# Kernel optimization log

Measured on AMD Instinct MI355X. Metric: run time of the kernel, lower is better.

The kernel has to match this reference:

```python
import jax, jax.numpy as jnp
import numpy as np

N, T, FS, FD, GH, RH, E = 100000, 24, 32, 8, 32, 64, 3200000


def spmm(edge_row, edge_col, edge_val, X):
    # out[i] = sum_e val[e] * X[col[e]]  for edges with row[e]==i
    return jax.ops.segment_sum(edge_val[:, None] * X[edge_col], edge_row, num_segments=N)


def setup_inputs() -> dict:
    key = jax.random.key(0)
    ks = jax.random.split(key, 20)
    s = 0.05
    return {
        "X_static": jax.random.normal(ks[0], (N, FS), jnp.float32),
        "X_dyn_mean": jax.random.normal(ks[1], (T, N, FD), jnp.float32),
        "edge_row": jax.random.randint(ks[2], (E,), 0, N, jnp.int32),
        "edge_col": jax.random.randint(ks[3], (E,), 0, N, jnp.int32),
        "edge_val": jax.random.uniform(ks[4], (E,), jnp.float32),
        # GraphConv layers
        "g1_W": jax.random.normal(ks[5], (GH, FS), jnp.float32) * s,
        "g1_b": jnp.zeros((GH,), jnp.float32),
        "g2_W": jax.random.normal(ks[6], (GH, GH), jnp.float32) * s,
        "g2_b": jnp.zeros((GH,), jnp.float32),
        # GRU (PyTorch layout: 3H rows = [r, z, n])
        "W_ih": jax.random.normal(ks[7], (3 * RH, GH + FD), jnp.float32) * s,
        "W_hh": jax.random.normal(ks[8], (3 * RH, RH), jnp.float32) * s,
        "b_ih": jnp.zeros((3 * RH,), jnp.float32),
        "b_hh": jnp.zeros((3 * RH,), jnp.float32),
        # MLP head
        "h1_W": jax.random.normal(ks[9], (64, RH), jnp.float32) * s,
        "h1_b": jnp.zeros((64,), jnp.float32),
        "h2_W": jax.random.normal(ks[10], (1, 64), jnp.float32) * s,
        "h2_b": jnp.zeros((1,), jnp.float32),
    }


def reference(X_static, X_dyn_mean, edge_row, edge_col, edge_val,
              g1_W, g1_b, g2_W, g2_b, W_ih, W_hh, b_ih, b_hh,
              h1_W, h1_b, h2_W, h2_b):
    # GraphConv x2: linear then sparse A_hat @ Xw, ReLU
    h = jax.nn.relu(spmm(edge_row, edge_col, edge_val, X_static @ g1_W.T + g1_b))
    h = jax.nn.relu(spmm(edge_row, edge_col, edge_val, h @ g2_W.T + g2_b))  # (N, GH)

    # z_t = concat([h, X_dyn_mean[t]], -1); precompute input-gate projections
    z_seq = jnp.concatenate([jnp.broadcast_to(h[None], (T, N, GH)), X_dyn_mean], axis=-1)  # (T,N,GH+FD)
    gi_all = jnp.einsum('tnd,hd->tnh', z_seq, W_ih) + b_ih  # (T,N,3H)

    def step(hs, gi):
        gh = hs @ W_hh.T + b_hh
        i_r, i_z, i_n = jnp.split(gi, 3, axis=-1)
        h_r, h_z, h_n = jnp.split(gh, 3, axis=-1)
        r = jax.nn.sigmoid(i_r + h_r)
        zg = jax.nn.sigmoid(i_z + h_z)
        n = jnp.tanh(i_n + r * h_n)
        h_new = (1.0 - zg) * n + zg * hs
        return h_new, h_new

    h0 = jnp.zeros((N, RH), jnp.float32)
    _, out = jax.lax.scan(step, h0, gi_all)  # (T,N,RH)

    y = jax.nn.relu(out @ h1_W.T + h1_b)
    y = jax.nn.sigmoid(y @ h2_W.T + h2_b)[..., 0]  # (T,N)
    return y
```

## Files before the change

### kernel.cpp

```cpp
#include <hip/hip_runtime.h>
#include <math.h>

typedef short bf16x8_t __attribute__((ext_vector_type(8)));
typedef float f32x4_t  __attribute__((ext_vector_type(4)));

__device__ __forceinline__ float fast_rcp(float x) { return __builtin_amdgcn_rcpf(x); }
__device__ __forceinline__ float sigmoidf_(float x) {
  return fast_rcp(1.0f + __expf(-x));
}
__device__ __forceinline__ float tanhf_(float x) {
  return fmaf(-2.0f, fast_rcp(__expf(2.0f * x) + 1.0f), 1.0f);
}
__device__ __forceinline__ unsigned short f2bf(float f) {
  unsigned int u = __float_as_uint(f);
  unsigned int r = (u + 0x7fffu + ((u >> 16) & 1u)) >> 16;
  return (unsigned short)r;
}
__device__ __forceinline__ float bf2f(unsigned short u) {
  return __uint_as_float(((unsigned int)u) << 16);
}
__device__ __forceinline__ unsigned int cvt_pk_bf16(float a, float b) {
  unsigned int d;
  asm("v_cvt_pk_bf16_f32 %0, %1, %2" : "=v"(d) : "v"(a), "v"(b));
  return d;
}

template<bool RELU_IN, bool OUT_BF16>
__global__ __launch_bounds__(256) void lin32_kernel(
    const float* __restrict__ X, const float* __restrict__ W,
    const float* __restrict__ b, void* __restrict__ outp, int N)
{
  __shared__ float sW[32][33];
  __shared__ float sb[32];
  __shared__ float sX[8][33];
  const int tid = threadIdx.x;
  for (int i = tid; i < 1024; i += 256) sW[i >> 5][i & 31] = W[i];
  if (tid < 32) sb[tid] = b[tid];
  const int n0 = blockIdx.x * 8;
  {
    float v = X[(size_t)n0 * 32 + tid];
    if (RELU_IN) v = fmaxf(v, 0.0f);
    sX[tid >> 5][tid & 31] = v;
  }
  __syncthreads();
  const int ln = tid >> 5, f = tid & 31;
  float acc = sb[f];
  #pragma unroll
  for (int j = 0; j < 32; j++) acc += sX[ln][j] * sW[f][j];
  if (OUT_BF16) ((unsigned short*)outp)[(size_t)n0 * 32 + tid] = f2bf(acc);
  else          ((float*)outp)[(size_t)n0 * 32 + tid] = acc;
}

__global__ __launch_bounds__(256) void spmm_kernel(
    const int* __restrict__ erow, const int* __restrict__ ecol,
    const float* __restrict__ eval, const float* __restrict__ X,
    float* __restrict__ out, int E)
{
  const long gid = (long)blockIdx.x * 256 + threadIdx.x;
  const int e = (int)(gid >> 3);
  const int q = (int)(gid & 7);
  if (e >= E) return;
  const int r = erow[e], c = ecol[e];
  const float v = eval[e];
  const float4 x = *(const float4*)(X + (size_t)c * 32 + q * 4);
  float* o = out + (size_t)r * 32 + q * 4;
  atomicAdd(o + 0, v * x.x);
  atomicAdd(o + 1, v * x.y);
  atomicAdd(o + 2, v * x.z);
  atomicAdd(o + 3, v * x.w);
}

#define BROWS 128
#define BSHIFT 7
#define EPB 4096
#define MAXBUCKETS 1024

__global__ __launch_bounds__(256) void lin_hist_k(
    const float* __restrict__ X, const float* __restrict__ W,
    const float* __restrict__ b, unsigned short* __restrict__ outp,
    int N, int linBlocks,
    const int* __restrict__ erow, int* __restrict__ blockHist,
    int* __restrict__ blockCnt, int E, int nBuckets)
{
  __shared__ float sW[32][33];
  __shared__ float sb[32];
  __shared__ float sX[8][33];
  __shared__ int h[MAXBUCKETS];
  const int tid = threadIdx.x;
  if ((int)blockIdx.x < linBlocks) {
    for (int i = tid; i < 1024; i += 256) sW[i >> 5][i & 31] = W[i];
    if (tid < 32) sb[tid] = b[tid];
    const int n0 = blockIdx.x * 8;
    sX[tid >> 5][tid & 31] = X[(size_t)n0 * 32 + tid];
    __syncthreads();
    const int ln = tid >> 5, f = tid & 31;
    float acc = sb[f];
    #pragma unroll
    for (int j = 0; j < 32; j++) acc += sX[ln][j] * sW[f][j];
    outp[(size_t)n0 * 32 + tid] = f2bf(acc);
  } else {
    const int bid = blockIdx.x - linBlocks;
    for (int i = tid; i < nBuckets; i += 256) h[i] = 0;
    __syncthreads();
    const int e0 = bid * EPB;
    const int cnt = min(E - e0, EPB);
    for (int i = tid; i < cnt; i += 256)
      atomicAdd(&h[erow[e0 + i] >> BSHIFT], 1);
    __syncthreads();
    int* o = blockHist + (size_t)bid * nBuckets;
    int* c = blockCnt + (size_t)bid * nBuckets;
    for (int i = tid; i < nBuckets; i += 256) { int v = h[i]; o[i] = v; c[i] = v; }
  }
}

__global__ __launch_bounds__(128) void colscan_k(
    int* __restrict__ blockHist, int* __restrict__ bucketTotal,
    int nb, int nBuckets)
{
  __shared__ int s[128];
  const int b = blockIdx.x;
  const int t = threadIdx.x;
  const int k = (nb + 127) >> 7;
  const int i0 = t * k, i1 = min(nb, i0 + k);
  int p = 0;
  for (int i = i0; i < i1; i++) p += blockHist[(size_t)i * nBuckets + b];
  s[t] = p;
  __syncthreads();
  #pragma unroll
  for (int off = 1; off < 128; off <<= 1) {
    int u = (t >= off) ? s[t - off] : 0;
    __syncthreads(); s[t] += u; __syncthreads();
  }
  int run = s[t] - p;
  if (t == 127) bucketTotal[b] = s[127];
  for (int i = i0; i < i1; i++) {
    int* q = &blockHist[(size_t)i * nBuckets + b];
    int v = *q;
    *q = run;
    run += v;
  }
}

__global__ __launch_bounds__(1024) void bucketstart_k(
    const int* __restrict__ bucketTotal, int* __restrict__ bucketStart,
    int nBuckets)
{
  __shared__ int s[1024];
  const int b = threadIdx.x;
  int v = (b < nBuckets) ? bucketTotal[b] : 0;
  s[b] = v;
  __syncthreads();
  for (int off = 1; off < 1024; off <<= 1) {
    int u = (b >= off) ? s[b - off] : 0;
    __syncthreads(); s[b] += u; __syncthreads();
  }
  if (b < nBuckets) bucketStart[b] = s[b] - v;
  if (b == nBuckets - 1) bucketStart[nBuckets] = s[b];
}

__global__ __launch_bounds__(256) void scatter_stage_k(
    const int* __restrict__ erow, const int* __restrict__ ecol,
    const float* __restrict__ evl, const int* __restrict__ blockOfs,
    const int* __restrict__ blockCnt,
    const int* __restrict__ bucketStart, int2* __restrict__ binned,
    int E, int nBuckets)
{
  __shared__ int2 rec[EPB];
  __shared__ unsigned short dstv[EPB];
  __shared__ int  cur[MAXBUCKETS];
  __shared__ int  gb[MAXBUCKETS];
  __shared__ int  part[256];
  const int tid = threadIdx.x;
  const int e0 = blockIdx.x * EPB;
  const int cntE = min(E - e0, EPB);
  const int* ofs = blockOfs + (size_t)blockIdx.x * nBuckets;
  const int* cnr = blockCnt + (size_t)blockIdx.x * nBuckets;

  for (int i = tid; i < nBuckets; i += 256) cur[i] = cnr[i];
  __syncthreads();

  const int k = (nBuckets + 255) >> 8;
  const int i0 = tid * k, i1 = min(i0 + k, nBuckets);
  int s = 0;
  for (int i = i0; i < i1; i++) s += cur[i];
  part[tid] = s;
  __syncthreads();
  for (int off = 1; off < 256; off <<= 1) {
    int u = (tid >= off) ? part[tid - off] : 0;
    __syncthreads(); part[tid] += u; __syncthreads();
  }
  int run = part[tid] - s;
  for (int i = i0; i < i1; i++) {
    int hv = cur[i];
    gb[i] = bucketStart[i] + ofs[i] - run;
    cur[i] = run;
    run += hv;
  }
  __syncthreads();

  for (int i = tid; i < cntE; i += 256) {
    int r = erow[e0 + i];
    int c = ecol[e0 + i];
    float v = evl[e0 + i];
    int b = r >> BSHIFT;
    int p = atomicAdd(&cur[b], 1);
    rec[p]  = make_int2(((r & (BROWS - 1)) << 17) | c, __float_as_int(v));
    dstv[p] = (unsigned short)b;
  }
  __syncthreads();

  for (int i = tid; i < cntE; i += 256)
    binned[gb[dstv[i]] + i] = rec[i];
}

__global__ __launch_bounds__(512) void bucket_sort_k(
    const int* __restrict__ bucketStart, const int2* __restrict__ binned,
    int2* __restrict__ pairs, int* __restrict__ startv, int* __restrict__ cnt,
    int N)
{
  __shared__ int h[BROWS], sc[BROWS], cur[BROWS];
  const int tid = threadIdx.x;
  const int bkt = blockIdx.x;
  const int s = bucketStart[bkt], e = bucketStart[bkt + 1];
  if (tid < BROWS) h[tid] = 0;
  __syncthreads();
  for (int i = s + tid; i < e; i += 512)
    atomicAdd(&h[((unsigned)binned[i].x) >> 17], 1);
  __syncthreads();
  if (tid < BROWS) sc[tid] = h[tid];
  __syncthreads();
  #pragma unroll
  for (int off = 1; off < BROWS; off <<= 1) {
    int u = (tid < BROWS && tid >= off) ? sc[tid - off] : 0;
    __syncthreads();
    if (tid < BROWS) sc[tid] += u;
    __syncthreads();
  }
  if (tid < BROWS) {
    int start = s + sc[tid] - h[tid];
    cur[tid] = start;
    int row = (bkt << BSHIFT) + tid;
    if (row < N) { startv[row] = start; cnt[row] = h[tid]; }
  }
  __syncthreads();
  for (int i = s + tid; i < e; i += 512) {
    int2 r = binned[i];
    int p = atomicAdd(&cur[((unsigned)r.x) >> 17], 1);
    pairs[p] = make_int2(r.x & 0x1ffff, r.y);
  }
}

__global__ __launch_bounds__(256) void hist_k(const int* __restrict__ erow, int* cnt, int E) {
  int e = blockIdx.x * 256 + threadIdx.x;
  if (e < E) atomicAdd(&cnt[erow[e]], 1);
}

__global__ __launch_bounds__(256) void scan1_k(const int* __restrict__ cnt, int* startv, int* bsum, int N) {
  __shared__ int s[256];
  int t = threadIdx.x, i = blockIdx.x * 256 + t;
  int v = (i < N) ? cnt[i] : 0;
  s[t] = v; __syncthreads();
  for (int off = 1; off < 256; off <<= 1) {
    int u = (t >= off) ? s[t - off] : 0;
    __syncthreads(); s[t] += u; __syncthreads();
  }
  if (i < N) startv[i] = s[t] - v;
  if (t == 255) bsum[blockIdx.x] = s[255];
}

__global__ __launch_bounds__(512) void scan2_k(const int* __restrict__ bsum, int* bsumx, int nb) {
  __shared__ int s[512];
  int t = threadIdx.x;
  int v = (t < nb) ? bsum[t] : 0;
  s[t] = v; __syncthreads();
  for (int off = 1; off < 512; off <<= 1) {
    int u = (t >= off) ? s[t - off] : 0;
    __syncthreads(); s[t] += u; __syncthreads();
  }
  if (t < nb) bsumx[t] = s[t] - v;
}

__global__ __launch_bounds__(256) void scan3_k(int* startv, const int* __restrict__ bsumx, int* cursor, int N) {
  int i = blockIdx.x * 256 + threadIdx.x;
  if (i < N) {
    int v = startv[i] + bsumx[i >> 8];
    startv[i] = v;
    cursor[i] = v;
  }
}

__global__ __launch_bounds__(256) void scatter_k(
    const int* __restrict__ erow, const int* __restrict__ ecol,
    const float* __restrict__ evl, int* cursor, int2* __restrict__ pairs, int E)
{
  int e = blockIdx.x * 256 + threadIdx.x;
  if (e < E) {
    int r = erow[e];
    int p = atomicAdd(&cursor[r], 1);
    pairs[p] = make_int2(ecol[e], __float_as_int(evl[e]));
  }
}

template<bool FUSE_LIN>
__global__ __launch_bounds__(256) void spmm_csr_bf16_k(
    const int* __restrict__ startv, const int* __restrict__ cnt,
    const int2* __restrict__ pairs, const unsigned short* __restrict__ X,
    void* __restrict__ outp, const float* __restrict__ W,
    const float* __restrict__ b, int N)
{
  __shared__ float sW[32][33];
  __shared__ float sb[32];
  __shared__ float sAcc[4][32];
  const int tid = threadIdx.x;
  if (FUSE_LIN) {
    for (int i = tid; i < 1024; i += 256) sW[i >> 5][i & 31] = W[i];
    if (tid < 32) sb[tid] = b[tid];
    __syncthreads();
  }
  int row = blockIdx.x * 4 + (tid >> 6);
  if (row >= N) return;
  int lane = tid & 63;
  int f = lane & 31, hh = lane >> 5;
  int start = startv[row];
  int len = cnt[row];
  int half = len >> 1;
  int base = start + (hh ? half : 0);
  int n = hh ? (len - half) : half;
  float acc = 0.0f;
  int i = 0;
  for (; i + 7 < n; i += 8) {
    int2 p0 = pairs[base + i + 0];
    int2 p1 = pairs[base + i + 1];
    int2 p2 = pairs[base + i + 2];
    int2 p3 = pairs[base + i + 3];
    int2 p4 = pairs[base + i + 4];
    int2 p5 = pairs[base + i + 5];
    int2 p6 = pairs[base + i + 6];
    int2 p7 = pairs[base + i + 7];
    float x0 = bf2f(X[(size_t)p0.x * 32 + f]);
    float x1 = bf2f(X[(size_t)p1.x * 32 + f]);
    float x2 = bf2f(X[(size_t)p2.x * 32 + f]);
    float x3 = bf2f(X[(size_t)p3.x * 32 + f]);
    float x4 = bf2f(X[(size_t)p4.x * 32 + f]);
    float x5 = bf2f(X[(size_t)p5.x * 32 + f]);
    float x6 = bf2f(X[(size_t)p6.x * 32 + f]);
    float x7 = bf2f(X[(size_t)p7.x * 32 + f]);
    acc = fmaf(__int_as_float(p0.y), x0, acc);
    acc = fmaf(__int_as_float(p1.y), x1, acc);
    acc = fmaf(__int_as_float(p2.y), x2, acc);
    acc = fmaf(__int_as_float(p3.y), x3, acc);
    acc = fmaf(__int_as_float(p4.y), x4, acc);
    acc = fmaf(__int_as_float(p5.y), x5, acc);
    acc = fmaf(__int_as_float(p6.y), x6, acc);
    acc = fmaf(__int_as_float(p7.y), x7, acc);
  }
  for (; i + 3 < n; i += 4) {
    int2 p0 = pairs[base + i + 0];
    int2 p1 = pairs[base + i + 1];
    int2 p2 = pairs[base + i + 2];
    int2 p3 = pairs[base + i + 3];
    float x0 = bf2f(X[(size_t)p0.x * 32 + f]);
    float x1 = bf2f(X[(size_t)p1.x * 32 + f]);
    float x2 = bf2f(X[(size_t)p2.x * 32 + f]);
    float x3 = bf2f(X[(size_t)p3.x * 32 + f]);
    acc = fmaf(__int_as_float(p0.y), x0, acc);
    acc = fmaf(__int_as_float(p1.y), x1, acc);
    acc = fmaf(__int_as_float(p2.y), x2, acc);
    acc = fmaf(__int_as_float(p3.y), x3, acc);
  }
  for (; i < n; i++) {
    int2 p = pairs[base + i];
    acc = fmaf(__int_as_float(p.y), bf2f(X[(size_t)p.x * 32 + f]), acc);
  }
  acc += __shfl_down(acc, 32);
  if (!FUSE_LIN) {
    if (hh == 0) ((float*)outp)[(size_t)row * 32 + f] = acc;
  } else {
    const int w = tid >> 6;
    if (hh == 0) sAcc[w][f] = fmaxf(acc, 0.0f);
    float part = 0.0f;
    #pragma unroll
    for (int j0 = 0; j0 < 16; j0++) {
      int j = hh * 16 + j0;
      part = fmaf(sAcc[w][j], sW[f][j], part);
    }
    part += __shfl_down(part, 32);
    if (hh == 0)
      ((unsigned short*)outp)[(size_t)row * 32 + f] = f2bf(sb[f] + part);
  }
}

#define NB 32

__global__ __launch_bounds__(256, 2) void gru_head_mfma(
    const float* __restrict__ acc2,
    const float* __restrict__ xdyn,
    const float* __restrict__ Wih,
    const float* __restrict__ Whh,
    const float* __restrict__ bih, const float* __restrict__ bhh,
    const float* __restrict__ h1W,
    const float* __restrict__ h1b, const float* __restrict__ h2W,
    const float* __restrict__ h2b,
    float* __restrict__ out, int N, int T)
{
  __shared__ __align__(16) unsigned short z[2][NB][104];
  __shared__ float s_red[2][NB][5];

  const int tid  = threadIdx.x;
  const int w    = tid >> 6;
  const int lane = tid & 63;
  const int ml   = lane & 15;
  const int q    = lane >> 4;
  const int n0   = blockIdx.x * NB;

  bf16x8_t A_r[3], A_z[3], A_in, A_hn[2];
  {
    const int j = 16 * w + ml;
    #pragma unroll
    for (int s = 0; s < 3; s++) {
      union { bf16x8_t v; unsigned short u[8]; } tr, tz;
      #pragma unroll
      for (int jj = 0; jj < 8; jj++) {
        int k = s * 32 + q * 8 + jj;
        float vr = (k < 64) ? Whh[j * 64 + k]        : (k < 72 ? Wih[j * 40 + 32 + (k - 64)] : 0.0f);
        float vz = (k < 64) ? Whh[(64 + j) * 64 + k] : (k < 72 ? Wih[(64 + j) * 40 + 32 + (k - 64)] : 0.0f);
        tr.u[jj] = f2bf(vr);
        tz.u[jj] = f2bf(vz);
      }
      A_r[s] = tr.v; A_z[s] = tz.v;
    }
    union { bf16x8_t v; unsigned short u[8]; } ti;
    #pragma unroll
    for (int jj = 0; jj < 8; jj++) {
      int kk = q * 8 + jj;
      ti.u[jj] = f2bf((kk < 8) ? Wih[(128 + j) * 40 + 32 + kk] : 0.0f);
    }
    A_in = ti.v;
    #pragma unroll
    for (int s = 0; s < 2; s++) {
      union { bf16x8_t v; unsigned short u[8]; } th;
      #pragma unroll
      for (int jj = 0; jj < 8; jj++)
        th.u[jj] = f2bf(Whh[(128 + j) * 64 + s * 32 + q * 8 + jj]);
      A_hn[s] = th.v;
    }
  }
  bf16x8_t Ah[2];
  #pragma unroll
  for (int s = 0; s < 2; s++) {
    union { bf16x8_t v; unsigned short u[8]; } tmp;
    #pragma unroll
    for (int jj = 0; jj < 8; jj++)
      tmp.u[jj] = f2bf(h1W[(16 * w + ml) * 64 + s * 32 + q * 8 + jj]);
    Ah[s] = tmp.v;
  }

  f32x4_t bhhn4, h1b4;
  float h2w_r[4];
  #pragma unroll
  for (int reg = 0; reg < 4; reg++) {
    int j = 16 * w + 4 * q + reg;
    bhhn4[reg] = bhh[128 + j];
    h1b4[reg]  = h1b[j];
    h2w_r[reg] = h2W[j];
  }
  const float h2b0 = h2b[0];

  {
    int nd = tid >> 3, f0 = (tid & 7) * 4;
    float4 v = *(const float4*)(acc2 + (size_t)(n0 + nd) * 32 + f0);
    uint2 pk;
    pk.x = cvt_pk_bf16(fmaxf(v.x, 0.0f), fmaxf(v.y, 0.0f));
    pk.y = cvt_pk_bf16(fmaxf(v.z, 0.0f), fmaxf(v.w, 0.0f));
    *(uint2*)&z[0][nd][f0] = pk;
  }
  __syncthreads();

  f32x4_t gis[3][2];
  {
    bf16x8_t Ag[3];
    #pragma unroll
    for (int g = 0; g < 3; g++) {
      union { bf16x8_t v; unsigned short u[8]; } tmp;
      #pragma unroll
      for (int jj = 0; jj < 8; jj++)
        tmp.u[jj] = f2bf(Wih[(g * 64 + 16 * w + ml) * 40 + q * 8 + jj]);
      Ag[g] = tmp.v;
    }
    bf16x8_t Bg[2];
    #pragma unroll
    for (int nt = 0; nt < 2; nt++)
      Bg[nt] = *(const bf16x8_t*)&z[0][nt * 16 + ml][q * 8];
    f32x4_t zero = {0.0f, 0.0f, 0.0f, 0.0f};
    #pragma unroll
    for (int g = 0; g < 3; g++)
      #pragma unroll
      for (int nt = 0; nt < 2; nt++)
        gis[g][nt] = __builtin_amdgcn_mfma_f32_16x16x32_bf16(Ag[g], Bg[nt], zero, 0, 0, 0);
  }
  __syncthreads();

  for (int i = tid; i < 2 * NB * 104 / 2; i += 256) ((unsigned int*)z)[i] = 0;
  #pragma unroll
  for (int reg = 0; reg < 4; reg++) {
    int j = 16 * w + 4 * q + reg;
    float br = bih[j] + bhh[j];
    float bz = bih[64 + j] + bhh[64 + j];
    float bn = bih[128 + j];
    #pragma unroll
    for (int nt = 0; nt < 2; nt++) {
      gis[0][nt][reg] += br;
      gis[1][nt][reg] += bz;
      gis[2][nt][reg] += bn;
    }
  }
  __syncthreads();

  float hreg[2][4] = {{0, 0, 0, 0}, {0, 0, 0, 0}};

  float4 xv = make_float4(0.f, 0.f, 0.f, 0.f);
  if (tid < 64) xv = *(const float4*)(xdyn + (size_t)n0 * 8 + tid * 4);

  for (int t = 0; t < T; t++) {
    const int b = t & 1;
    if (tid < 64) {
      uint2 pk;
      pk.x = cvt_pk_bf16(xv.x, xv.y);
      pk.y = cvt_pk_bf16(xv.z, xv.w);
      *(uint2*)&z[b][tid >> 1][64 + (tid & 1) * 4] = pk;
      if (t + 1 < T)
        xv = *(const float4*)(xdyn + ((size_t)(t + 1) * N + n0) * 8 + tid * 4);
    }
    __syncthreads();

    if (t >= 2 && tid < 32) {
      float s = s_red[1 - b][tid][0] + s_red[1 - b][tid][1] +
                s_red[1 - b][tid][2] + s_red[1 - b][tid][3];
      out[(size_t)(t - 2) * N + n0 + tid] = sigmoidf_(s + h2b0);
    }

    #pragma unroll
    for (int nt = 0; nt < 2; nt++) {
      bf16x8_t B0 = *(const bf16x8_t*)&z[b][nt * 16 + ml][q * 8];
      bf16x8_t B1 = *(const bf16x8_t*)&z[b][nt * 16 + ml][32 + q * 8];
      bf16x8_t B2 = *(const bf16x8_t*)&z[b][nt * 16 + ml][64 + q * 8];

      f32x4_t ar  = gis[0][nt];
      f32x4_t az  = gis[1][nt];
      f32x4_t ain = gis[2][nt];
      f32x4_t ahn = bhhn4;
      ar  = __builtin_amdgcn_mfma_f32_16x16x32_bf16(A_r[0], B0, ar, 0, 0, 0);
      az  = __builtin_amdgcn_mfma_f32_16x16x32_bf16(A_z[0], B0, az, 0, 0, 0);
      ahn = __builtin_amdgcn_mfma_f32_16x16x32_bf16(A_hn[0], B0, ahn, 0, 0, 0);
      ar  = __builtin_amdgcn_mfma_f32_16x16x32_bf16(A_r[1], B1, ar, 0, 0, 0);
      az  = __builtin_amdgcn_mfma_f32_16x16x32_bf16(A_z[1], B1, az, 0, 0, 0);
      ahn = __builtin_amdgcn_mfma_f32_16x16x32_bf16(A_hn[1], B1, ahn, 0, 0, 0);
      ar  = __builtin_amdgcn_mfma_f32_16x16x32_bf16(A_r[2], B2, ar, 0, 0, 0);
      az  = __builtin_amdgcn_mfma_f32_16x16x32_bf16(A_z[2], B2, az, 0, 0, 0);
      ain = __builtin_amdgcn_mfma_f32_16x16x32_bf16(A_in,  B2, ain, 0, 0, 0);

      if (t >= 1) {
        f32x4_t ha = h1b4;
        ha = __builtin_amdgcn_mfma_f32_16x16x32_bf16(Ah[0], B0, ha, 0, 0, 0);
        ha = __builtin_amdgcn_mfma_f32_16x16x32_bf16(Ah[1], B1, ha, 0, 0, 0);
        float p = 0.0f;
        #pragma unroll
        for (int reg = 0; reg < 4; reg++)
          p += h2w_r[reg] * fmaxf(ha[reg], 0.0f);
        p += __shfl_xor(p, 16, 64);
        p += __shfl_xor(p, 32, 64);
        if (q == 0) s_red[b][nt * 16 + ml][w] = p;
      }

      float hv[4];
      #pragma unroll
      for (int reg = 0; reg < 4; reg++) {
        float r  = sigmoidf_(ar[reg]);
        float zg = sigmoidf_(az[reg]);
        float nn = tanhf_(fmaf(r, ahn[reg], ain[reg]));
        float h  = fmaf(zg, hreg[nt][reg] - nn, nn);
        hreg[nt][reg] = h;
        hv[reg] = h;
      }
      uint2 pk;
      pk.x = cvt_pk_bf16(hv[0], hv[1]);
      pk.y = cvt_pk_bf16(hv[2], hv[3]);
      *(uint2*)&z[1 - b][nt * 16 + ml][16 * w + 4 * q] = pk;
    }
  }

  const int bl = (T - 1) & 1;
  __syncthreads();

  if (tid < 32) {
    float s = s_red[bl][tid][0] + s_red[bl][tid][1] +
              s_red[bl][tid][2] + s_red[bl][tid][3];
    out[(size_t)(T - 2) * N + n0 + tid] = sigmoidf_(s + h2b0);
  }
  #pragma unroll
  for (int nt = 0; nt < 2; nt++) {
    bf16x8_t B0 = *(const bf16x8_t*)&z[1 - bl][nt * 16 + ml][q * 8];
    bf16x8_t B1 = *(const bf16x8_t*)&z[1 - bl][nt * 16 + ml][32 + q * 8];
    f32x4_t ha = h1b4;
    ha = __builtin_amdgcn_mfma_f32_16x16x32_bf16(Ah[0], B0, ha, 0, 0, 0);
    ha = __builtin_amdgcn_mfma_f32_16x16x32_bf16(Ah[1], B1, ha, 0, 0, 0);
    float p = 0.0f;
    #pragma unroll
    for (int reg = 0; reg < 4; reg++)
      p += h2w_r[reg] * fmaxf(ha[reg], 0.0f);
    p += __shfl_xor(p, 16, 64);
    p += __shfl_xor(p, 32, 64);
    if (q == 0) s_red[1 - bl][nt * 16 + ml][w] = p;
  }
  __syncthreads();
  if (tid < 32) {
    float s = s_red[1 - bl][tid][0] + s_red[1 - bl][tid][1] +
              s_red[1 - bl][tid][2] + s_red[1 - bl][tid][3];
    out[(size_t)(T - 1) * N + n0 + tid] = sigmoidf_(s + h2b0);
  }
}

extern "C" void kernel_launch(void* const* d_in, const int* in_sizes, int n_in,
                              void* d_out, int out_size, void* d_ws, size_t ws_size,
                              hipStream_t stream) {
  const float* Xs   = (const float*)d_in[0];
  const float* Xd   = (const float*)d_in[1];
  const int*   erow = (const int*)d_in[2];
  const int*   ecol = (const int*)d_in[3];
  const float* evl  = (const float*)d_in[4];
  const float* g1W  = (const float*)d_in[5];
  const float* g1b  = (const float*)d_in[6];
  const float* g2W  = (const float*)d_in[7];
  const float* g2b  = (const float*)d_in[8];
  const float* Wih  = (const float*)d_in[9];
  const float* Whh  = (const float*)d_in[10];
  const float* bih  = (const float*)d_in[11];
  const float* bhh  = (const float*)d_in[12];
  const float* h1W  = (const float*)d_in[13];
  const float* h1b  = (const float*)d_in[14];
  const float* h2W  = (const float*)d_in[15];
  const float* h2b  = (const float*)d_in[16];

  const int N = in_sizes[0] / 32;
  const int E = in_sizes[2];
  const int T = in_sizes[1] / (N * 8);

  float* out  = (float*)d_out;
  char*  base = (char*)d_ws;
  float* buf0 = (float*)base;
  float* buf1 = buf0 + (size_t)N * 32;
  int*   cnt    = (int*)(buf1 + (size_t)N * 32);
  int*   startv = cnt + N;
  int*   cursor = startv + N;
  int*   bsum   = cursor + N;
  int*   bsumx  = bsum + 512;
  unsigned short* buf0h = (unsigned short*)buf0;
  unsigned short* buf1h = (unsigned short*)buf1;

  const int nBuckets = (N + BROWS - 1) >> BSHIFT;
  const int nbBin    = (E + EPB - 1) / EPB;

  int* bucketStart = bsumx + 512;
  int* bucketTotal = bucketStart + nBuckets + 1;
  int* blockHist   = bucketTotal + nBuckets;
  int* blockCnt    = blockHist + (size_t)nbBin * nBuckets;
  char* pp = (char*)(blockCnt + (size_t)nbBin * nBuckets);
  pp = (char*)(((uintptr_t)pp + 15) & ~(uintptr_t)15);
  int2* pairs  = (int2*)pp;
  int2* binned = pairs + E;

  const size_t neededA = (size_t)((char*)(binned + E) - base);
  const size_t neededB = (size_t)((char*)(pairs + E) - base);

  const int linBlocks = (N + 7) / 8;
  const int eBlocks   = (E + 255) / 256;
  const int nb1       = (N + 255) / 256;

  const bool tierA = (ws_size >= neededA) && (nBuckets <= MAXBUCKETS) &&
                     (N <= (1 << 17));
  const bool tierB = !tierA && (ws_size >= neededB);

  if (tierA) {
    lin_hist_k<<<linBlocks + nbBin, 256, 0, stream>>>(
        Xs, g1W, g1b, buf0h, N, linBlocks, erow, blockHist, blockCnt, E, nBuckets);

    colscan_k<<<nBuckets, 128, 0, stream>>>(blockHist, bucketTotal, nbBin, nBuckets);
    bucketstart_k<<<1, 1024, 0, stream>>>(bucketTotal, bucketStart, nBuckets);
    scatter_stage_k<<<nbBin, 256, 0, stream>>>(erow, ecol, evl, blockHist,
                                               blockCnt, bucketStart, binned,
                                               E, nBuckets);
    bucket_sort_k<<<nBuckets, 512, 0, stream>>>(bucketStart, binned, pairs,
                                                startv, cnt, N);

    spmm_csr_bf16_k<true><<<(N + 3) / 4, 256, 0, stream>>>(
        startv, cnt, pairs, buf0h, buf1h, g2W, g2b, N);
    spmm_csr_bf16_k<false><<<(N + 3) / 4, 256, 0, stream>>>(
        startv, cnt, pairs, buf1h, buf0, nullptr, nullptr, N);
  } else if (tierB) {
    lin32_kernel<false, true><<<linBlocks, 256, 0, stream>>>(Xs, g1W, g1b, buf0h, N);

    hipMemsetAsync(cnt, 0, (size_t)N * sizeof(int), stream);
    hist_k<<<eBlocks, 256, 0, stream>>>(erow, cnt, E);
    scan1_k<<<nb1, 256, 0, stream>>>(cnt, startv, bsum, N);
    scan2_k<<<1, 512, 0, stream>>>(bsum, bsumx, nb1);
    scan3_k<<<nb1, 256, 0, stream>>>(startv, bsumx, cursor, N);
    scatter_k<<<eBlocks, 256, 0, stream>>>(erow, ecol, evl, cursor, pairs, E);

    spmm_csr_bf16_k<true><<<(N + 3) / 4, 256, 0, stream>>>(
        startv, cnt, pairs, buf0h, buf1h, g2W, g2b, N);
    spmm_csr_bf16_k<false><<<(N + 3) / 4, 256, 0, stream>>>(
        startv, cnt, pairs, buf1h, buf0, nullptr, nullptr, N);
  } else {
    lin32_kernel<false, false><<<linBlocks, 256, 0, stream>>>(Xs, g1W, g1b, buf1, N);
    const int spmmBlocks = (int)(((long)E * 8 + 255) / 256);
    hipMemsetAsync(buf0, 0, (size_t)N * 32 * sizeof(float), stream);
    spmm_kernel<<<spmmBlocks, 256, 0, stream>>>(erow, ecol, evl, buf1, buf0, E);
    lin32_kernel<true, false><<<linBlocks, 256, 0, stream>>>(buf0, g2W, g2b, buf1, N);
    hipMemsetAsync(buf0, 0, (size_t)N * 32 * sizeof(float), stream);
    spmm_kernel<<<spmmBlocks, 256, 0, stream>>>(erow, ecol, evl, buf1, buf0, E);
  }

  gru_head_mfma<<<N / NB, 256, 0, stream>>>(buf0, Xd, Wih, Whh, bih, bhh,
                                            h1W, h1b, h2W, h2b, out, N, T);
}
```

Before: 571.8 us.

## Replace per-block column scan with atomic bucket cursors and drop bucketstart kernel

Removes the column-wise exclusive scan over per-block histograms and the single-block bucket-start kernel. Bucket totals come from a simple column sum. Each scatter block now computes bucket starts itself and reserves its slice within each bucket through a global atomic cursor. bucket_sort_k recomputes its bucket start by reducing the preceding totals. This cuts one launch and a write-back pass over the histogram, but makes the order within a bucket nondeterministic and repeats prefix work in every block.

```diff
diff --git a/kernel.cpp b/kernel.cpp
--- a/kernel.cpp
+++ b/kernel.cpp
@@ -79,8 +79,8 @@
     const float* __restrict__ X, const float* __restrict__ W,
     const float* __restrict__ b, unsigned short* __restrict__ outp,
     int N, int linBlocks,
-    const int* __restrict__ erow, int* __restrict__ blockHist,
-    int* __restrict__ blockCnt, int E, int nBuckets)
+    const int* __restrict__ erow, int* __restrict__ blockCnt,
+    int E, int nBuckets)
 {
   __shared__ float sW[32][33];
   __shared__ float sb[32];
@@ -107,63 +107,35 @@
     for (int i = tid; i < cnt; i += 256)
       atomicAdd(&h[erow[e0 + i] >> BSHIFT], 1);
     __syncthreads();
-    int* o = blockHist + (size_t)bid * nBuckets;
     int* c = blockCnt + (size_t)bid * nBuckets;
-    for (int i = tid; i < nBuckets; i += 256) { int v = h[i]; o[i] = v; c[i] = v; }
-  }
-}
-
-__global__ __launch_bounds__(128) void colscan_k(
-    int* __restrict__ blockHist, int* __restrict__ bucketTotal,
-    int nb, int nBuckets)
+    for (int i = tid; i < nBuckets; i += 256) c[i] = h[i];
+  }
+}
+
+__global__ __launch_bounds__(128) void colsum_k(
+    const int* __restrict__ blockCnt, int* __restrict__ bucketTotal,
+    int* __restrict__ auxCur, int nb, int nBuckets)
 {
   __shared__ int s[128];
   const int b = blockIdx.x;
   const int t = threadIdx.x;
-  const int k = (nb + 127) >> 7;
-  const int i0 = t * k, i1 = min(nb, i0 + k);
   int p = 0;
-  for (int i = i0; i < i1; i++) p += blockHist[(size_t)i * nBuckets + b];
+  for (int i = t; i < nb; i += 128) p += blockCnt[(size_t)i * nBuckets + b];
   s[t] = p;
   __syncthreads();
   #pragma unroll
-  for (int off = 1; off < 128; off <<= 1) {
-    int u = (t >= off) ? s[t - off] : 0;
-    __syncthreads(); s[t] += u; __syncthreads();
-  }
-  int run = s[t] - p;
-  if (t == 127) bucketTotal[b] = s[127];
-  for (int i = i0; i < i1; i++) {
-    int* q = &blockHist[(size_t)i * nBuckets + b];
-    int v = *q;
-    *q = run;
-    run += v;
-  }
-}
-
-__global__ __launch_bounds__(1024) void bucketstart_k(
-    const int* __restrict__ bucketTotal, int* __restrict__ bucketStart,
-    int nBuckets)
-{
-  __shared__ int s[1024];
-  const int b = threadIdx.x;
-  int v = (b < nBuckets) ? bucketTotal[b] : 0;
-  s[b] = v;
-  __syncthreads();
-  for (int off = 1; off < 1024; off <<= 1) {
-    int u = (b >= off) ? s[b - off] : 0;
-    __syncthreads(); s[b] += u; __syncthreads();
-  }
-  if (b < nBuckets) bucketStart[b] = s[b] - v;
-  if (b == nBuckets - 1) bucketStart[nBuckets] = s[b];
+  for (int off = 64; off > 0; off >>= 1) {
+    if (t < off) s[t] += s[t + off];
+    __syncthreads();
+  }
+  if (t == 0) { bucketTotal[b] = s[0]; auxCur[b] = 0; }
 }
 
 __global__ __launch_bounds__(256) void scatter_stage_k(
     const int* __restrict__ erow, const int* __restrict__ ecol,
-    const float* __restrict__ evl, const int* __restrict__ blockOfs,
-    const int* __restrict__ blockCnt,
-    const int* __restrict__ bucketStart, int2* __restrict__ binned,
-    int E, int nBuckets)
+    const float* __restrict__ evl, const int* __restrict__ blockCnt,
+    const int* __restrict__ bucketTotal, int* __restrict__ auxCur,
+    int2* __restrict__ binned, int E, int nBuckets)
 {
   __shared__ int2 rec[EPB];
   __shared__ unsigned short dstv[EPB];
@@ -173,7 +145,6 @@
   const int tid = threadIdx.x;
   const int e0 = blockIdx.x * EPB;
   const int cntE = min(E - e0, EPB);
-  const int* ofs = blockOfs + (size_t)blockIdx.x * nBuckets;
   const int* cnr = blockCnt + (size_t)blockIdx.x * nBuckets;
 
   for (int i = tid; i < nBuckets; i += 256) cur[i] = cnr[i];
@@ -181,20 +152,43 @@
 
   const int k = (nBuckets + 255) >> 8;
   const int i0 = tid * k, i1 = min(i0 + k, nBuckets);
-  int s = 0;
-  for (int i = i0; i < i1; i++) s += cur[i];
-  part[tid] = s;
-  __syncthreads();
-  for (int off = 1; off < 256; off <<= 1) {
-    int u = (tid >= off) ? part[tid - off] : 0;
-    __syncthreads(); part[tid] += u; __syncthreads();
-  }
-  int run = part[tid] - s;
-  for (int i = i0; i < i1; i++) {
-    int hv = cur[i];
-    gb[i] = bucketStart[i] + ofs[i] - run;
-    cur[i] = run;
-    run += hv;
+
+  {
+    int s = 0;
+    for (int i = i0; i < i1; i++) s += bucketTotal[i];
+    part[tid] = s;
+    __syncthreads();
+    for (int off = 1; off < 256; off <<= 1) {
+      int u = (tid >= off) ? part[tid - off] : 0;
+      __syncthreads(); part[tid] += u; __syncthreads();
+    }
+    int run = part[tid] - s;
+    for (int i = i0; i < i1; i++) {
+      gb[i] = run;
+      run += bucketTotal[i];
+    }
+  }
+  __syncthreads();
+
+  {
+    int s = 0;
+    for (int i = i0; i < i1; i++) s += cur[i];
+    part[tid] = s;
+    __syncthreads();
+    for (int off = 1; off < 256; off <<= 1) {
+      int u = (tid >= off) ? part[tid - off] : 0;
+      __syncthreads(); part[tid] += u; __syncthreads();
+    }
+    int run = part[tid] - s;
+    for (int i = i0; i < i1; i++) {
+      int c  = cur[i];
+      int ls = run;
+      run += c;
+      int base = 0;
+      if (c > 0) base = gb[i] + atomicAdd(&auxCur[i], c);
+      gb[i]  = base - ls;
+      cur[i] = ls;
+    }
   }
   __syncthreads();
 
@@ -214,14 +208,27 @@
 }
 
 __global__ __launch_bounds__(512) void bucket_sort_k(
-    const int* __restrict__ bucketStart, const int2* __restrict__ binned,
+    const int* __restrict__ bucketTotal, const int2* __restrict__ binned,
     int2* __restrict__ pairs, int* __restrict__ startv, int* __restrict__ cnt,
     int N)
 {
   __shared__ int h[BROWS], sc[BROWS], cur[BROWS];
+  __shared__ int red[512];
   const int tid = threadIdx.x;
   const int bkt = blockIdx.x;
-  const int s = bucketStart[bkt], e = bucketStart[bkt + 1];
+  {
+    int acc = 0;
+    for (int i = tid; i < bkt; i += 512) acc += bucketTotal[i];
+    red[tid] = acc;
+    __syncthreads();
+    #pragma unroll
+    for (int off = 256; off > 0; off >>= 1) {
+      if (tid < off) red[tid] += red[tid + off];
+      __syncthreads();
+    }
+  }
+  const int s = red[0];
+  const int e = s + bucketTotal[bkt];
   if (tid < BROWS) h[tid] = 0;
   __syncthreads();
   for (int i = s + tid; i < e; i += 512)
@@ -660,10 +667,9 @@
   const int nBuckets = (N + BROWS - 1) >> BSHIFT;
   const int nbBin    = (E + EPB - 1) / EPB;
 
-  int* bucketStart = bsumx + 512;
-  int* bucketTotal = bucketStart + nBuckets + 1;
-  int* blockHist   = bucketTotal + nBuckets;
-  int* blockCnt    = blockHist + (size_t)nbBin * nBuckets;
+  int* bucketTotal = bsumx + 512;
+  int* auxCur      = bucketTotal + nBuckets;
+  int* blockCnt    = auxCur + nBuckets;
   char* pp = (char*)(blockCnt + (size_t)nbBin * nBuckets);
   pp = (char*)(((uintptr_t)pp + 15) & ~(uintptr_t)15);
   int2* pairs  = (int2*)pp;
@@ -682,14 +688,16 @@
 
   if (tierA) {
     lin_hist_k<<<linBlocks + nbBin, 256, 0, stream>>>(
-        Xs, g1W, g1b, buf0h, N, linBlocks, erow, blockHist, blockCnt, E, nBuckets);
-
-    colscan_k<<<nBuckets, 128, 0, stream>>>(blockHist, bucketTotal, nbBin, nBuckets);
-    bucketstart_k<<<1, 1024, 0, stream>>>(bucketTotal, bucketStart, nBuckets);
-    scatter_stage_k<<<nbBin, 256, 0, stream>>>(erow, ecol, evl, blockHist,
-                                               blockCnt, bucketStart, binned,
+        Xs, g1W, g1b, buf0h, N, linBlocks, erow, blockCnt, E, nBuckets);
+
+    colsum_k<<<nBuckets, 128, 0, stream>>>(blockCnt, bucketTotal, auxCur,
+                                           nbBin, nBuckets);
+
+    scatter_stage_k<<<nbBin, 256, 0, stream>>>(erow, ecol, evl, blockCnt,
+                                               bucketTotal, auxCur, binned,
                                                E, nBuckets);
-    bucket_sort_k<<<nBuckets, 512, 0, stream>>>(bucketStart, binned, pairs,
+
+    bucket_sort_k<<<nBuckets, 512, 0, stream>>>(bucketTotal, binned, pairs,
                                                 startv, cnt, N);
 
     spmm_csr_bf16_k<true><<<(N + 3) / 4, 256, 0, stream>>>(
```

Result: slower. 629.4 us (+10.1%).
